# Kernel tuning notes

Measured on AMD Instinct MI355X. Metric: run time of the kernel, lower is better.

## Reference

```python
import jax, jax.numpy as jnp
import numpy as np

N, C, T, V = 64, 256, 64, 25

def setup_inputs() -> dict:
    key = jax.random.key(0)
    ks = jax.random.split(key, 11)
    inp = {
        't': jax.random.uniform(ks[0], (1,), dtype=jnp.float32),
        'x': jax.random.normal(ks[1], (N, C, T, V), dtype=jnp.float32),
        'A': jax.random.normal(ks[2], (V, V), dtype=jnp.float32) * 0.2,
    }
    for i in range(4):
        inp[f'w{i+1}'] = jax.random.normal(ks[3 + 2 * i], (C, C), dtype=jnp.float32) * (1.0 / np.sqrt(C))
        inp[f'b{i+1}'] = jax.random.normal(ks[4 + 2 * i], (C,), dtype=jnp.float32) * 0.02
    return inp


def _block(res, A, w, b):
    # graph diffusion over joint dim: A[v,u] @ x[n,c,t,u]
    y = jnp.einsum('vu,nctu->nctv', A, res)
    # 1x1 conv == pointwise channel GEMM
    y = jnp.einsum('oc,nctv->notv', w, y) + b[None, :, None, None]
    return jax.nn.relu(y + res)


def reference(t, x, A, w1, b1, w2, b2, w3, b3, w4, b4):
    # t is unused by the ODE function body (autonomous dynamics)
    res = _block(x, A, w1, b1)
    res = _block(res, A, w2, b2)
    res = _block(res, A, w3, b3)
    res = _block(res, A, w4, b4)
    return res
```

## Files before the change

kernel.cpp:

```cpp
#include <hip/hip_runtime.h>
#include <math.h>

#define NN 64
#define CC 256
#define TT 64
#define VV 25

typedef __bf16 bf16;
typedef __attribute__((ext_vector_type(8)))  __bf16 bf16x8;
typedef __attribute__((ext_vector_type(16))) float  f32x16;
typedef __attribute__((ext_vector_type(4)))  unsigned int uint4v;

#define RST 266

#define OFF_S0    0
#define OFF_S1    17024
#define OFF_SAB   34048
#define OFF_SBIAS 36096
#define SMEM_BYTES 40192

__global__ void convert_w(const float* __restrict__ w1, const float* __restrict__ w2,
                          const float* __restrict__ w3, const float* __restrict__ w4,
                          bf16* __restrict__ wp) {
    const int gid = blockIdx.x * 256 + threadIdx.x;
    const int e8  = gid * 8;
    const int blk = e8 >> 16;
    const int off = e8 & 65535;
    const int row = off >> 8;
    const int col = off & 255;
    const float* src = (blk == 0) ? w1 : (blk == 1) ? w2 : (blk == 2) ? w3 : w4;
    const float4 f0 = *(const float4*)(src + off);
    const float4 f1 = *(const float4*)(src + off + 4);
    bf16x8 o;
    o[0] = (bf16)f0.x; o[1] = (bf16)f0.y; o[2] = (bf16)f0.z; o[3] = (bf16)f0.w;
    o[4] = (bf16)f1.x; o[5] = (bf16)f1.y; o[6] = (bf16)f1.z; o[7] = (bf16)f1.w;
    const int wv = row >> 6, pair = (row >> 5) & 1, l31 = row & 31;
    const int k = col >> 4, lh = (col >> 3) & 1;
    wp += (((size_t)(blk * 4 + wv) * 16 + k) * 1024) + pair * 512 + (lh * 32 + l31) * 8;
    *(bf16x8*)wp = o;
}

#define MFMA(A, B, C) __builtin_amdgcn_mfma_f32_32x32x16_bf16(A, B, C, 0, 0, 0)

static __device__ __forceinline__ unsigned int pkbf(float a, float b) {
    unsigned short lo = __builtin_bit_cast(unsigned short, (__bf16)a);
    unsigned short hi = __builtin_bit_cast(unsigned short, (__bf16)b);
    return (unsigned int)lo | ((unsigned int)hi << 16);
}

__global__ __launch_bounds__(256, 4) void ode_mfma(
    const float* __restrict__ x, const float* __restrict__ Amat,
    const bf16* __restrict__ wp,
    const float* __restrict__ b1, const float* __restrict__ b2,
    const float* __restrict__ b3, const float* __restrict__ b4,
    float* __restrict__ out)
{
    __shared__ __attribute__((aligned(16))) char smem[SMEM_BYTES];
    bf16*  s0    = (bf16*)(smem + OFF_S0);
    bf16*  s1    = (bf16*)(smem + OFF_S1);
    bf16*  sAb   = (bf16*)(smem + OFF_SAB);
    float* sbias = (float*)(smem + OFF_SBIAS);

    const int t    = blockIdx.x;
    const int n    = blockIdx.y;
    const int tid  = threadIdx.x;
    const int wave = tid >> 6;
    const int lane = tid & 63;
    const int lh   = lane >> 5;
    const int l31  = lane & 31;
    const int o0   = wave * 64;

    bf16x8 wA[4], wB[4];
    {
        const bf16* wb0 = wp + ((size_t)wave * 16) * 1024 + lane * 8;
        #pragma unroll
        for (int q = 0; q < 4; ++q) {
            wA[q] = *(const bf16x8*)(wb0 + q * 1024);
            wB[q] = *(const bf16x8*)(wb0 + q * 1024 + 512);
        }
    }

    sbias[0 * CC + tid] = b1[tid];
    sbias[1 * CC + tid] = b2[tid];
    sbias[2 * CC + tid] = b3[tid];
    sbias[3 * CC + tid] = b4[tid];

    for (int i = tid; i < 32 * 32; i += 256) {
        const int v = i >> 5, u = i & 31;
        sAb[i] = (v < VV && u < VV) ? (bf16)Amat[v * VV + u] : (bf16)0.f;
    }

    for (int i = tid; i < 7 * 256; i += 256) {
        const int r = 25 + (i >> 8), c = i & 255;
        s0[r * RST + c] = (bf16)0.f;
        s1[r * RST + c] = (bf16)0.f;
    }

    {
        const float* xb = x + ((size_t)n * CC * TT + t) * VV;
        for (int i = tid; i < CC * VV; i += 256) {
            const int c = i / VV;
            const int v = i - c * VV;
            s0[v * RST + c] = (bf16)xb[(size_t)c * TT * VV + v];
        }
    }
    __syncthreads();

    const bf16x8 bfA0 = *(const bf16x8*)&sAb[l31 * 32 + lh * 8];
    const bf16x8 bfA1 = *(const bf16x8*)&sAb[l31 * 32 + 16 + lh * 8];

    for (int blk = 0; blk < 4; ++blk) {
        bf16* rd = (blk & 1) ? s1 : s0;
        bf16* wr = (blk & 1) ? s0 : s1;
        const bf16* wbase = wp + ((size_t)(blk * 4 + wave) * 16) * 1024 + lane * 8;

        f32x16 z0 = {}, z1 = {};
        bf16x8 af[2];
        af[0] = *(const bf16x8*)&rd[l31 * RST + lh * 8];
        #pragma unroll
        for (int k = 0; k < 16; ++k) {
            if (k < 15)
                af[(k + 1) & 1] = *(const bf16x8*)&rd[l31 * RST + (k + 1) * 16 + lh * 8];
            const bf16x8 a = af[k & 1];
            z0 = MFMA(a, wA[k & 3], z0);
            z1 = MFMA(a, wB[k & 3], z1);
            if (k + 4 < 16) {
                wA[k & 3] = *(const bf16x8*)(wbase + (k + 4) * 1024);
                wB[k & 3] = *(const bf16x8*)(wbase + (k + 4) * 1024 + 512);
            }
        }

        if (blk < 3) {
            const bf16* wn = wp + ((size_t)((blk + 1) * 4 + wave) * 16) * 1024 + lane * 8;
            #pragma unroll
            for (int q = 0; q < 4; ++q) {
                wA[q] = *(const bf16x8*)(wn + q * 1024);
                wB[q] = *(const bf16x8*)(wn + q * 1024 + 512);
            }
        }

        #define FINAL_TILE(ZZ, TL)                                                  \
        {                                                                           \
            unsigned int a0 = pkbf(ZZ[0],  ZZ[1]),  a1 = pkbf(ZZ[2],  ZZ[3]);       \
            unsigned int a2 = pkbf(ZZ[4],  ZZ[5]),  a3 = pkbf(ZZ[6],  ZZ[7]);       \
            unsigned int a4 = pkbf(ZZ[8],  ZZ[9]),  a5 = pkbf(ZZ[10], ZZ[11]);      \
            unsigned int a6 = pkbf(ZZ[12], ZZ[13]), a7 = pkbf(ZZ[14], ZZ[15]);      \
            asm("v_permlane32_swap_b32 %0, %1" : "+v"(a0), "+v"(a2));               \
            asm("v_permlane32_swap_b32 %0, %1" : "+v"(a1), "+v"(a3));               \
            asm("v_permlane32_swap_b32 %0, %1" : "+v"(a4), "+v"(a6));               \
            asm("v_permlane32_swap_b32 %0, %1" : "+v"(a5), "+v"(a7));               \
            const bf16x8 y0 = __builtin_bit_cast(bf16x8, (uint4v){a0, a1, a2, a3}); \
            const bf16x8 y1 = __builtin_bit_cast(bf16x8, (uint4v){a4, a5, a6, a7}); \
            f32x16 d = {};                                                          \
            d = MFMA(bfA0, y0, d);                                                  \
            d = MFMA(bfA1, y1, d);                                                  \
            const int o = o0 + (TL) * 32 + l31;                                     \
            const float bb = sbias[blk * CC + o];                                   \
            _Pragma("unroll")                                                       \
            for (int q = 0; q < 16; ++q) {                                          \
                const int v = (q & 3) + 8 * (q >> 2) + 4 * lh;                      \
                float val = d[q] + bb + (float)rd[v * RST + o];                     \
                val = fmaxf(val, 0.f);                                              \
                if (v < VV) {                                                       \
                    if (blk < 3) wr[v * RST + o] = (bf16)val;                       \
                    else out[(((size_t)n * CC + o) * TT + t) * VV + v] = val;       \
                }                                                                   \
            }                                                                       \
        }
        FINAL_TILE(z0, 0)
        FINAL_TILE(z1, 1)
        #undef FINAL_TILE

        if (blk < 3) __syncthreads();
    }
}

extern "C" void kernel_launch(void* const* d_in, const int* in_sizes, int n_in,
                              void* d_out, int out_size, void* d_ws, size_t ws_size,
                              hipStream_t stream) {
    const float* x  = (const float*)d_in[1];
    const float* A  = (const float*)d_in[2];
    const float* w1 = (const float*)d_in[3];
    const float* b1 = (const float*)d_in[4];
    const float* w2 = (const float*)d_in[5];
    const float* b2 = (const float*)d_in[6];
    const float* w3 = (const float*)d_in[7];
    const float* b3 = (const float*)d_in[8];
    const float* w4 = (const float*)d_in[9];
    const float* b4 = (const float*)d_in[10];
    float* out = (float*)d_out;
    bf16* wp = (bf16*)d_ws;

    convert_w<<<128, 256, 0, stream>>>(w1, w2, w3, w4, wp);
    dim3 grid(TT, NN);
    ode_mfma<<<grid, 256, 0, stream>>>(x, A, wp, b1, b2, b3, b4, out);
}
```

Before: 365.0 us.

## Process two time slices per block to reuse weight fragments across both

Result: slower. 388.7 us (+6.5%).

```diff
diff --git a/kernel.cpp b/kernel.cpp
--- a/kernel.cpp
+++ b/kernel.cpp
@@ -13,8 +13,8 @@
 
 #define RST 266
 
-#define OFF_S0    0
-#define OFF_S1    17024
+#define OFF_SA    0
+#define OFF_SB    17024
 #define OFF_SAB   34048
 #define OFF_SBIAS 36096
 #define SMEM_BYTES 40192
@@ -48,7 +48,7 @@
     return (unsigned int)lo | ((unsigned int)hi << 16);
 }
 
-__global__ __launch_bounds__(256, 4) void ode_mfma(
+__global__ __launch_bounds__(256, 3) void ode_mfma(
     const float* __restrict__ x, const float* __restrict__ Amat,
     const bf16* __restrict__ wp,
     const float* __restrict__ b1, const float* __restrict__ b2,
@@ -56,12 +56,13 @@
     float* __restrict__ out)
 {
     __shared__ __attribute__((aligned(16))) char smem[SMEM_BYTES];
-    bf16*  s0    = (bf16*)(smem + OFF_S0);
-    bf16*  s1    = (bf16*)(smem + OFF_S1);
+    bf16*  sA    = (bf16*)(smem + OFF_SA);
+    bf16*  sB    = (bf16*)(smem + OFF_SB);
     bf16*  sAb   = (bf16*)(smem + OFF_SAB);
     float* sbias = (float*)(smem + OFF_SBIAS);
 
-    const int t    = blockIdx.x;
+    const int t0   = blockIdx.x * 2;
+    const int t1   = t0 + 1;
     const int n    = blockIdx.y;
     const int tid  = threadIdx.x;
     const int wave = tid >> 6;
@@ -92,16 +93,18 @@
 
     for (int i = tid; i < 7 * 256; i += 256) {
         const int r = 25 + (i >> 8), c = i & 255;
-        s0[r * RST + c] = (bf16)0.f;
-        s1[r * RST + c] = (bf16)0.f;
+        sA[r * RST + c] = (bf16)0.f;
+        sB[r * RST + c] = (bf16)0.f;
     }
 
     {
-        const float* xb = x + ((size_t)n * CC * TT + t) * VV;
+        const float* xb = x + ((size_t)n * CC * TT + t0) * VV;
         for (int i = tid; i < CC * VV; i += 256) {
             const int c = i / VV;
             const int v = i - c * VV;
-            s0[v * RST + c] = (bf16)xb[(size_t)c * TT * VV + v];
+            const float* p = xb + (size_t)c * TT * VV + v;
+            sA[v * RST + c] = (bf16)p[0];
+            sB[v * RST + c] = (bf16)p[VV];
         }
     }
     __syncthreads();
@@ -110,25 +113,33 @@
     const bf16x8 bfA1 = *(const bf16x8*)&sAb[l31 * 32 + 16 + lh * 8];
 
     for (int blk = 0; blk < 4; ++blk) {
-        bf16* rd = (blk & 1) ? s1 : s0;
-        bf16* wr = (blk & 1) ? s0 : s1;
         const bf16* wbase = wp + ((size_t)(blk * 4 + wave) * 16) * 1024 + lane * 8;
 
-        f32x16 z0 = {}, z1 = {};
-        bf16x8 af[2];
-        af[0] = *(const bf16x8*)&rd[l31 * RST + lh * 8];
+        f32x16 zA0 = {}, zA1 = {}, zB0 = {}, zB1 = {};
+        bf16x8 afA[4], afB[4];
+        afA[0] = *(const bf16x8*)&sA[l31 * RST + lh * 8];
+        afB[0] = *(const bf16x8*)&sB[l31 * RST + lh * 8];
+        afA[1] = *(const bf16x8*)&sA[l31 * RST + 16 + lh * 8];
+        afB[1] = *(const bf16x8*)&sB[l31 * RST + 16 + lh * 8];
+
         #pragma unroll
         for (int k = 0; k < 16; ++k) {
-            if (k < 15)
-                af[(k + 1) & 1] = *(const bf16x8*)&rd[l31 * RST + (k + 1) * 16 + lh * 8];
-            const bf16x8 a = af[k & 1];
-            z0 = MFMA(a, wA[k & 3], z0);
-            z1 = MFMA(a, wB[k & 3], z1);
+            if (k + 2 < 16) {
+                afA[(k + 2) & 3] = *(const bf16x8*)&sA[l31 * RST + (k + 2) * 16 + lh * 8];
+                afB[(k + 2) & 3] = *(const bf16x8*)&sB[l31 * RST + (k + 2) * 16 + lh * 8];
+            }
+            const bf16x8 aA = afA[k & 3];
+            const bf16x8 aB = afB[k & 3];
+            zA0 = MFMA(aA, wA[k & 3], zA0);
+            zB0 = MFMA(aB, wA[k & 3], zB0);
+            zA1 = MFMA(aA, wB[k & 3], zA1);
+            zB1 = MFMA(aB, wB[k & 3], zB1);
             if (k + 4 < 16) {
                 wA[k & 3] = *(const bf16x8*)(wbase + (k + 4) * 1024);
                 wB[k & 3] = *(const bf16x8*)(wbase + (k + 4) * 1024 + 512);
             }
         }
+        __syncthreads();
 
         if (blk < 3) {
             const bf16* wn = wp + ((size_t)((blk + 1) * 4 + wave) * 16) * 1024 + lane * 8;
@@ -139,7 +150,7 @@
             }
         }
 
-        #define FINAL_TILE(ZZ, TL)                                                  \
+        #define FINAL_TILE(ZZ, SBUF, TSL, TL)                                       \
         {                                                                           \
             unsigned int a0 = pkbf(ZZ[0],  ZZ[1]),  a1 = pkbf(ZZ[2],  ZZ[3]);       \
             unsigned int a2 = pkbf(ZZ[4],  ZZ[5]),  a3 = pkbf(ZZ[6],  ZZ[7]);       \
@@ -159,16 +170,18 @@
             _Pragma("unroll")                                                       \
             for (int q = 0; q < 16; ++q) {                                          \
                 const int v = (q & 3) + 8 * (q >> 2) + 4 * lh;                      \
-                float val = d[q] + bb + (float)rd[v * RST + o];                     \
+                float val = d[q] + bb + (float)SBUF[v * RST + o];                   \
                 val = fmaxf(val, 0.f);                                              \
                 if (v < VV) {                                                       \
-                    if (blk < 3) wr[v * RST + o] = (bf16)val;                       \
-                    else out[(((size_t)n * CC + o) * TT + t) * VV + v] = val;       \
+                    if (blk < 3) SBUF[v * RST + o] = (bf16)val;                     \
+                    else out[(((size_t)n * CC + o) * TT + (TSL)) * VV + v] = val;   \
                 }                                                                   \
             }                                                                       \
         }
-        FINAL_TILE(z0, 0)
-        FINAL_TILE(z1, 1)
+        FINAL_TILE(zA0, sA, t0, 0)
+        FINAL_TILE(zA1, sA, t0, 1)
+        FINAL_TILE(zB0, sB, t1, 0)
+        FINAL_TILE(zB1, sB, t1, 1)
         #undef FINAL_TILE
 
         if (blk < 3) __syncthreads();
@@ -192,6 +205,6 @@
     bf16* wp = (bf16*)d_ws;
 
     convert_w<<<128, 256, 0, stream>>>(w1, w2, w3, w4, wp);
-    dim3 grid(TT, NN);
+    dim3 grid(TT / 2, NN);
     ode_mfma<<<grid, 256, 0, stream>>>(x, A, wp, b1, b2, b3, b4, out);
 }
```
